# Kernel tuning notes

Measured on AMD Instinct MI355X. Metric: run time of the kernel, lower is better.

Reference implementation:

```python
import jax, jax.numpy as jnp
import numpy as np
from jax import lax

B, H, W, CL, CC, CD, NH, NP = 8, 48, 48, 384, 384, 384, 12, 4
N = H * W
HD = CL // NH
SCALE = HD ** -0.5


def _pool_mat(n, out=7):
    # torch AdaptiveAvgPool2d bin edges: [floor(i*n/out), ceil((i+1)*n/out))
    M = np.zeros((out, n), np.float32)
    for i in range(out):
        s = (i * n) // out
        e = -(-((i + 1) * n) // out)
        M[i, s:e] = 1.0 / (e - s)
    return jnp.asarray(M)


def _resize_mat(out_n, in_n):
    # bilinear, align_corners=False (torch F.interpolate)
    M = np.zeros((out_n, in_n), np.float32)
    scale = in_n / out_n
    for o in range(out_n):
        src = (o + 0.5) * scale - 0.5
        src = min(max(src, 0.0), in_n - 1.0)
        i0 = int(np.floor(src))
        i1 = min(i0 + 1, in_n - 1)
        f = src - i0
        M[o, i0] += 1.0 - f
        M[o, i1] += f
    return jnp.asarray(M)


def _ln_c(x, g, b):
    # LayerNorm over channel dim of NCHW, eps=1e-6
    mu = jnp.mean(x, axis=1, keepdims=True)
    var = jnp.mean((x - mu) ** 2, axis=1, keepdims=True)
    xn = (x - mu) * lax.rsqrt(var + 1e-6)
    return xn * g[None, :, None, None] + b[None, :, None, None]


def _c1(x, w):
    # 1x1 conv, w: (out,in)
    return jnp.einsum('oc,bchw->bohw', w, x)


def _bilerp(feat, grid):
    # feat (G,C,Hs,Ws), grid (G,M,2) xy in [-1,1]; align_corners=False, zero padding
    G, C, Hs, Ws = feat.shape
    x = (grid[..., 0] + 1.0) * 0.5 * Ws - 0.5
    y = (grid[..., 1] + 1.0) * 0.5 * Hs - 0.5
    x0 = jnp.floor(x)
    y0 = jnp.floor(y)
    fx = x - x0
    fy = y - y0
    featf = feat.transpose(0, 2, 3, 1).reshape(G, Hs * Ws, C)
    x0i = x0.astype(jnp.int32)
    y0i = y0.astype(jnp.int32)

    def corner(ix, iy):
        valid = ((ix >= 0) & (ix < Ws) & (iy >= 0) & (iy < Hs)).astype(feat.dtype)
        flat = jnp.clip(iy, 0, Hs - 1) * Ws + jnp.clip(ix, 0, Ws - 1)
        g = jax.vmap(lambda f, i: f[i])(featf, flat)  # (G,M,C)
        return g * valid[..., None]

    v00 = corner(x0i, y0i)
    v01 = corner(x0i + 1, y0i)
    v10 = corner(x0i, y0i + 1)
    v11 = corner(x0i + 1, y0i + 1)
    w00 = ((1 - fx) * (1 - fy))[..., None]
    w01 = (fx * (1 - fy))[..., None]
    w10 = ((1 - fx) * fy)[..., None]
    w11 = (fx * fy)[..., None]
    return v00 * w00 + v01 * w01 + v10 * w10 + v11 * w11  # (G,M,C)


def _forward(local_feat, context_prior, deformable_x, W_q, W_k, W_v, W_pre, ln1_g, ln1_b,
             W_post, dw_w, dw_b, ln2_g, ln2_b, W_lo, b_lo, W_off, b_off,
             attention_biases, W_p, bn_g, bn_b, bn_mean, bn_var):
    q = _c1(local_feat, W_q)  # (B,CL,H,W)

    # context_offset_guide: 1x1 -> GELU -> adaptive pool 7x7 -> LN(C) -> 1x1 to 32 -> resize
    cg = jax.nn.gelu(_c1(context_prior, W_pre), approximate=False)
    Mh, Mw = _pool_mat(H), _pool_mat(W)
    pooled = jnp.einsum('oh,pw,bchw->bcop', Mh, Mw, cg)
    guide = _c1(_ln_c(pooled, ln1_g, ln1_b), W_post)  # (B,32,7,7)
    Uh, Uw = _resize_mat(H, 7), _resize_mat(W, 7)
    guide = jnp.einsum('Oh,Pw,bchw->bcOP', Uh, Uw, guide)  # (B,32,H,W)

    # local_offset_base: dwconv3x3 -> LN(C) -> GELU -> 1x1 to 32
    dw = lax.conv_general_dilated(local_feat, dw_w, (1, 1), [(1, 1), (1, 1)],
                                  dimension_numbers=('NCHW', 'OIHW', 'NCHW'),
                                  feature_group_count=CL) + dw_b[None, :, None, None]
    lo = jax.nn.gelu(_ln_c(dw, ln2_g, ln2_b), approximate=False)
    lo = _c1(lo, W_lo) + b_lo[None, :, None, None]  # (B,32,H,W)

    fused = jnp.concatenate([guide, lo], axis=1)  # (B,64,H,W)
    off = _c1(fused, W_off) + b_off[None, :, None, None]  # (B,NH*NP*2,H,W)
    off = off.transpose(0, 2, 3, 1).reshape(B, H, W, NH, NP, 2)
    offn = off / jnp.asarray([W, H], dtype=off.dtype)

    ry = (jnp.arange(H, dtype=off.dtype) + 0.5) / H
    rx = (jnp.arange(W, dtype=off.dtype) + 0.5) / W
    ref = jnp.stack([jnp.broadcast_to(rx[None, :], (H, W)),
                     jnp.broadcast_to(ry[:, None], (H, W))], axis=-1)  # (H,W,2) xy
    grid = (ref[None, :, :, None, None, :] + offn) * 2.0 - 1.0  # (B,H,W,NH,NP,2)

    gridh = grid.reshape(B, N, NH, NP, 2).transpose(0, 2, 1, 3, 4)  # (B,NH,N,NP,2)
    grid_r = gridh.reshape(B * NH, N * NP, 2)

    k = _c1(context_prior, W_k).reshape(B * NH, HD, H, W)
    v = _c1(deformable_x, W_v).reshape(B * NH, HD, H, W)
    k_s = _bilerp(k, grid_r).reshape(B, NH, N, NP, HD)
    v_s = _bilerp(v, grid_r).reshape(B, NH, N, NP, HD)

    qh = q.reshape(B, NH, HD, N).transpose(0, 1, 3, 2)  # (B,NH,N,HD)
    scores = jnp.einsum('bhnd,bhnpd->bhnp', qh, k_s) * SCALE

    # relative position bias: idx(p1,p2) = |dy|*W + |dx| (first-seen enumeration)
    px = jnp.clip(jnp.round((gridh[..., 0] + 1.0) * 0.5 * W - 0.5), 0, W - 1).astype(jnp.int32)
    py = jnp.clip(jnp.round((gridh[..., 1] + 1.0) * 0.5 * H - 0.5), 0, H - 1).astype(jnp.int32)
    n = jnp.arange(N, dtype=jnp.int32)
    qy = (n // W)[None, None, :, None]
    qx = (n % W)[None, None, :, None]
    bidx = jnp.abs(qy - py) * W + jnp.abs(qx - px)  # (B,NH,N,NP)
    bias = attention_biases[jnp.arange(NH)[None, :, None, None], bidx]

    attn = jax.nn.softmax(scores + bias, axis=-1)
    out = jnp.einsum('bhnp,bhnpd->bhnd', attn, v_s)  # (B,NH,N,HD)
    out = out.transpose(0, 1, 3, 2).reshape(B, CL, H, W)

    y = _c1(out, W_p)
    y = bn_g[None, :, None, None] * (y - bn_mean[None, :, None, None]) * \
        lax.rsqrt(bn_var[None, :, None, None] + 1e-5) + bn_b[None, :, None, None]
    return y


def setup_inputs():
    ks = jax.random.split(jax.random.key(0), 16)
    f32 = jnp.float32
    d = {
        'local_feat': jax.random.normal(ks[0], (B, CL, H, W), f32),
        'context_prior': jax.random.normal(ks[1], (B, CC, H, W), f32),
        'deformable_x': jax.random.normal(ks[2], (B, CD, H, W), f32),
        'W_q': jax.random.normal(ks[3], (CL, CL), f32) * 0.02,
        'W_k': jax.random.normal(ks[4], (CL, CC), f32) * 0.02,
        'W_v': jax.random.normal(ks[5], (CD, CD), f32) * 0.02,
        'W_pre': jax.random.normal(ks[6], (CC, CC), f32) * 0.02,
        'ln1_g': jnp.ones((CC,), f32),
        'ln1_b': jnp.zeros((CC,), f32),
        'W_post': jax.random.normal(ks[7], (32, CC), f32) * 0.02,
        'dw_w': jax.random.normal(ks[8], (CL, 1, 3, 3), f32) * 0.1,
        'dw_b': jnp.zeros((CL,), f32),
        'ln2_g': jnp.ones((CL,), f32),
        'ln2_b': jnp.zeros((CL,), f32),
        'W_lo': jax.random.normal(ks[9], (32, CL), f32) * 0.02,
        'b_lo': jnp.zeros((32,), f32),
        'W_off': jax.random.normal(ks[10], (NH * NP * 2, 64), f32) * 0.01,
        'b_off': jax.random.normal(ks[11], (NH * NP * 2,), f32) * 0.5,
        'attention_biases': jax.random.normal(ks[12], (NH, H * W), f32) * 0.02,
        'W_p': jax.random.normal(ks[13], (CL, CL), f32) * 0.02,
        'bn_g': jnp.ones((CL,), f32),
        'bn_b': jnp.zeros((CL,), f32),
        'bn_mean': jax.random.normal(ks[14], (CL,), f32) * 0.01,
        'bn_var': jax.random.uniform(ks[15], (CL,), f32, 0.5, 1.5),
    }
    return d


def reference(local_feat, context_prior, deformable_x, W_q, W_k, W_v, W_pre, ln1_g, ln1_b,
              W_post, dw_w, dw_b, ln2_g, ln2_b, W_lo, b_lo, W_off, b_off,
              attention_biases, W_p, bn_g, bn_b, bn_mean, bn_var):
    return _forward(local_feat, context_prior, deformable_x, W_q, W_k, W_v, W_pre, ln1_g,
                    ln1_b, W_post, dw_w, dw_b, ln2_g, ln2_b, W_lo, b_lo, W_off, b_off,
                    attention_biases, W_p, bn_g, bn_b, bn_mean, bn_var)
```

## Files before the change

### kernel.cpp

```cpp
#include <hip/hip_runtime.h>
#include <hip/hip_bf16.h>
#include <math.h>

#define B_ 8
#define H_ 48
#define W_ 48
#define N_ 2304
#define C_ 384
#define NH_ 12
#define NP_ 4
#define HD_ 32
#define SCALE_ 0.17677669529663687f

typedef unsigned short ushort;
typedef short bf16x8 __attribute__((ext_vector_type(8)));
typedef float f32x4 __attribute__((ext_vector_type(4)));

__device__ __forceinline__ float b2f(ushort u) {
    union { float f; unsigned i; } x; x.i = ((unsigned)u) << 16; return x.f;
}
__device__ __forceinline__ ushort f2b(float f) {
    __hip_bfloat16 h = __float2bfloat16(f);
    return *(ushort*)&h;
}
__device__ __forceinline__ float ldin(const void* p, size_t i, int isbf) {
    return isbf ? b2f(((const ushort*)p)[i]) : ((const float*)p)[i];
}
__device__ __forceinline__ float geluf(float x) {
    return 0.5f * x * (1.0f + erff(x * 0.70710678118654752440f));
}
__device__ __forceinline__ int iabs(int x) { return x < 0 ? -x : x; }
__device__ __forceinline__ int get_isbf(const void* lnq) {
    return (*(const unsigned*)lnq == 0x3F803F80u) ? 1 : 0;
}

__device__ __forceinline__ void gl_lds16(const ushort* g, ushort* l) {
    __builtin_amdgcn_global_load_lds(
        (const __attribute__((address_space(1))) unsigned int*)g,
        (__attribute__((address_space(3))) unsigned int*)l, 16, 0, 0);
}

#define PREP_MAX 24
struct PrepTab {
    const void* src[PREP_MAX];
    void*       dst[PREP_MAX];
    int         n[PREP_MAX];
    int         tobf[PREP_MAX];
};
struct TPtrs { const void* src[3]; ushort* dst[3]; };
struct SetupRaw {
    const void* WoffRaw;
    const void* WloRaw;
    const void* bloRaw;
    const void* boffRaw;
    const void* dwRaw;
    const void* lnq;
    ushort* Bext;
    float*  biasp;
    float*  dwwT;
};

__global__ __launch_bounds__(256) void setup_kernel(TPtrs tp, PrepTab tab, int ne, SetupRaw rw)
{
    const int isbf = get_isbf(rw.lnq);
    const int tid = threadIdx.x;
    const int bid = blockIdx.x;
    const int DWT0 = ne * 8;
    const int WC0  = DWT0 + 2;
    const int T30  = WC0 + 96;

    if (bid < DWT0) {
        const int e = bid >> 3, sub = bid & 7;
        const int n = tab.n[e];
        const void* src = tab.src[e];
        if (tab.tobf[e]) {
            ushort* dst = (ushort*)tab.dst[e];
            if (isbf) {
                const ushort* s = (const ushort*)src;
                for (int i = sub * 256 + tid; i < n; i += 8 * 256) dst[i] = s[i];
            } else {
                const float* s = (const float*)src;
                for (int i = sub * 256 + tid; i < n; i += 8 * 256) dst[i] = f2b(s[i]);
            }
        } else {
            float* dst = (float*)tab.dst[e];
            if (isbf) {
                const ushort* s = (const ushort*)src;
                for (int i = sub * 256 + tid; i < n; i += 8 * 256) dst[i] = b2f(s[i]);
            } else {
                const float* s = (const float*)src;
                for (int i = sub * 256 + tid; i < n; i += 8 * 256) dst[i] = s[i];
            }
        }
    } else if (bid < WC0) {
        const int c = (bid - DWT0) * 256 + tid;
        if (c < C_) {
#pragma unroll
            for (int u = 0; u < 9; u++)
                rw.dwwT[u * C_ + c] = ldin(rw.dwRaw, (size_t)c * 9 + u, isbf);
        }
    } else if (bid < T30) {
        const int co = bid - WC0;
        for (int c = tid; c < C_; c += 256) {
            float acc = 0.f;
#pragma unroll 8
            for (int j = 0; j < 32; j++)
                acc += ldin(rw.WoffRaw, (size_t)co * 64 + 32 + j, isbf)
                     * ldin(rw.WloRaw, (size_t)j * 384 + c, isbf);
            ushort hi = f2b(acc);
            float r = acc - b2f(hi);
            ushort lo = f2b(r);
            rw.Bext[co * 1152 + c] = hi;
            rw.Bext[co * 1152 + 384 + c] = lo;
            rw.Bext[co * 1152 + 768 + c] = hi;
        }
        if (tid == 0) {
            float bp = ldin(rw.boffRaw, co, isbf);
            for (int j = 0; j < 32; j++)
                bp += ldin(rw.WoffRaw, (size_t)co * 64 + 32 + j, isbf)
                    * ldin(rw.bloRaw, j, isbf);
            rw.biasp[co] = bp;
        }
    } else {
        const int t3 = bid - T30;
        const int x = t3 % 36;
        const int rem = t3 / 36;
        const int y = rem % 12;
        const int z = rem / 12;
        const int which = z >> 3;
        const int b = z & 7;
        const int n0 = x * 64, c0 = y * 32;
        const void* in = tp.src[which];
        ushort* out = tp.dst[which];
        const int t = tid;

        __shared__ unsigned tile[64][33];

        if (isbf) {
            {
                const int c = t >> 3, s = t & 7;
                uint4 v = *(const uint4*)((const ushort*)in + ((size_t)b * C_ + c0 + c) * N_ + n0 + s * 8);
                const int nb = s * 8;
                tile[nb + 0][c] = v.x & 0xffff; tile[nb + 1][c] = v.x >> 16;
                tile[nb + 2][c] = v.y & 0xffff; tile[nb + 3][c] = v.y >> 16;
                tile[nb + 4][c] = v.z & 0xffff; tile[nb + 5][c] = v.z >> 16;
                tile[nb + 6][c] = v.w & 0xffff; tile[nb + 7][c] = v.w >> 16;
            }
            __syncthreads();
            {
                const int n = t >> 2, s = t & 3;
                const int cb = s * 8;
                unsigned p0 = tile[n][cb + 0] | (tile[n][cb + 1] << 16);
                unsigned p1 = tile[n][cb + 2] | (tile[n][cb + 3] << 16);
                unsigned p2 = tile[n][cb + 4] | (tile[n][cb + 5] << 16);
                unsigned p3 = tile[n][cb + 6] | (tile[n][cb + 7] << 16);
                uint4 o; o.x = p0; o.y = p1; o.z = p2; o.w = p3;
                *(uint4*)(out + ((size_t)b * N_ + n0 + n) * C_ + c0 + cb) = o;
            }
        } else {
            float* tf = (float*)&tile[0][0];
            const int tx = t & 31, ty = t >> 5;
            for (int sub = 0; sub < 2; sub++) {
                int ns = n0 + sub * 32;
                __syncthreads();
#pragma unroll
                for (int u = 0; u < 4; u++) {
                    int c = ty + u * 8;
                    tf[c * 33 + tx] = ((const float*)in)[((size_t)b * C_ + c0 + c) * N_ + ns + tx];
                }
                __syncthreads();
#pragma unroll
                for (int u = 0; u < 4; u++) {
                    int n = ty + u * 8;
                    out[((size_t)b * N_ + ns + n) * C_ + c0 + tx] = f2b(tf[tx * 33 + n]);
                }
            }
        }
    }
}

struct QKV4Ptrs { const ushort* A[4]; const ushort* Bw[4]; void* Y[4]; };
__global__ __launch_bounds__(256, 5) void mega_gemm_kernel(
    QKV4Ptrs qp,
    const ushort* __restrict__ AHI, const ushort* __restrict__ ALO,
    const ushort* __restrict__ Bext, float* __restrict__ OFFP)
{
    __shared__ ushort As[2][128 * 32];
    __shared__ ushort Bs[2][128 * 32];
    const int tid = threadIdx.x;
    const int lane = tid & 63, wave = tid >> 6;
    const int wr = wave >> 1, wc = wave & 1;
    const int quad = lane >> 4, l15 = lane & 15;
    const int bid = blockIdx.x;

    if (bid < 144) {
        const int m0 = bid * 128;

        f32x4 acc[4][3];
#pragma unroll
        for (int i = 0; i < 4; i++)
#pragma unroll
            for (int j = 0; j < 3; j++) acc[i][j] = (f32x4){0.f, 0.f, 0.f, 0.f};

        auto stage = [&](int p, int t) {
            const int seg = t / 12;
            const ushort* Ag = (seg < 2) ? AHI : ALO;
            const int acol = t * 32 - seg * 384;
            const int bcol = t * 32;
#pragma unroll
            for (int u = 0; u < 2; u++) {
                int idx = tid + 256 * u;
                int r = idx >> 2, s = idx & 3;
                int rb = r < 96 ? r : 95;
                gl_lds16(Ag + (size_t)(m0 + r) * 384 + acol + 8 * s, &As[p][idx * 8]);
                gl_lds16(Bext + (size_t)rb * 1152 + bcol + 8 * s, &Bs[p][idx * 8]);
            }
        };

        stage(0, 0);
        const int nt = 36;
        for (int t = 0; t < nt; ++t) {
            if (t + 1 < nt) {
                stage((t + 1) & 1, t + 1);
                asm volatile("s_waitcnt vmcnt(4)" ::: "memory");
            } else {
                asm volatile("s_waitcnt vmcnt(0)" ::: "memory");
            }
            __builtin_amdgcn_s_barrier();
            __builtin_amdgcn_sched_barrier(0);
            const int p = t & 1;
            bf16x8 af[4], bfr[3];
#pragma unroll
            for (int i = 0; i < 4; i++)
                af[i]  = *(const bf16x8*)&As[p][(wr * 64 + i * 16 + l15) * 32 + quad * 8];
#pragma unroll
            for (int j = 0; j < 3; j++)
                bfr[j] = *(const bf16x8*)&Bs[p][(wc * 48 + j * 16 + l15) * 32 + quad * 8];
#pragma unroll
            for (int i = 0; i < 4; i++)
#pragma unroll
                for (int j = 0; j < 3; j++)
                    acc[i][j] = __builtin_amdgcn_mfma_f32_16x16x32_bf16(af[i], bfr[j], acc[i][j], 0, 0, 0);
            __builtin_amdgcn_s_barrier();
        }

#pragma unroll
        for (int i = 0; i < 4; i++) {
#pragma unroll
            for (int r = 0; r < 4; r++) {
                int m = m0 + wr * 64 + i * 16 + quad * 4 + r;
#pragma unroll
                for (int j = 0; j < 3; j++) {
                    int co = wc * 48 + j * 16 + l15;
                    OFFP[(size_t)m * 96 + co] = acc[i][j][r];
                }
            }
        }
    } else {
        const int q = bid - 144;
        const int zc = q / 54, r2 = q % 54;
        const int which = zc >> 3, b = zc & 7;
        const int m0 = (r2 / 3) * 128;
        const int n0 = (r2 % 3) * 128;
        const ushort* Ag = qp.A[which];
        const ushort* Bg = qp.Bw[which];

        f32x4 acc[4][4];
#pragma unroll
        for (int i = 0; i < 4; i++)
#pragma unroll
            for (int j = 0; j < 4; j++) acc[i][j] = (f32x4){0.f, 0.f, 0.f, 0.f};

        const size_t abase = (size_t)b * (size_t)N_ * C_;

        auto stage = [&](int p, int kc) {
#pragma unroll
            for (int u = 0; u < 2; u++) {
                int idx = tid + 256 * u;
                int r = idx >> 2, s = idx & 3;
                gl_lds16(Ag + abase + (size_t)(m0 + r) * C_ + kc + 8 * s, &As[p][idx * 8]);
                gl_lds16(Bg + (size_t)(n0 + r) * C_ + kc + 8 * s, &Bs[p][idx * 8]);
            }
        };

        stage(0, 0);
        const int nt = C_ / 32;
        for (int t = 0; t < nt; ++t) {
            if (t + 1 < nt) {
                stage((t + 1) & 1, (t + 1) * 32);
                asm volatile("s_waitcnt vmcnt(4)" ::: "memory");
            } else {
                asm volatile("s_waitcnt vmcnt(0)" ::: "memory");
            }
            __builtin_amdgcn_s_barrier();
            __builtin_amdgcn_sched_barrier(0);
            const int p = t & 1;
            bf16x8 af[4], bfr[4];
#pragma unroll
            for (int i = 0; i < 4; i++)
                af[i]  = *(const bf16x8*)&As[p][(wr * 64 + i * 16 + l15) * 32 + quad * 8];
#pragma unroll
            for (int j = 0; j < 4; j++)
                bfr[j] = *(const bf16x8*)&Bs[p][(wc * 64 + j * 16 + l15) * 32 + quad * 8];
#pragma unroll
            for (int i = 0; i < 4; i++)
#pragma unroll
                for (int j = 0; j < 4; j++)
                    acc[i][j] = __builtin_amdgcn_mfma_f32_16x16x32_bf16(af[i], bfr[j], acc[i][j], 0, 0, 0);
            __builtin_amdgcn_s_barrier();
        }

        ushort* Yg = (ushort*)qp.Y[which];
        if (which < 3) {
#pragma unroll
            for (int i = 0; i < 4; i++) {
#pragma unroll
                for (int r = 0; r < 4; r++) {
                    int m = m0 + wr * 64 + i * 16 + quad * 4 + r;
#pragma unroll
                    for (int j = 0; j < 4; j++) {
                        int nn = n0 + wc * 64 + j * 16 + l15;
                        Yg[abase + (size_t)m * C_ + nn] = f2b(acc[i][j][r]);
                    }
                }
            }
        } else {
#pragma unroll
            for (int i = 0; i < 4; i++) {
#pragma unroll
                for (int r = 0; r < 4; r++) {
                    int m = m0 + wr * 64 + i * 16 + quad * 4 + r;
#pragma unroll
                    for (int j = 0; j < 4; j++) {
                        int nn = n0 + wc * 64 + j * 16 + l15;
                        Yg[abase + (size_t)m * C_ + nn] = f2b(geluf(acc[i][j][r]));
                    }
                }
            }
        }
    }
}

__global__ __launch_bounds__(256) void gemm_final_kernel(
    const ushort* __restrict__ WpB, const ushort* __restrict__ AOut,
    void* __restrict__ Yg,
    const float* __restrict__ bng, const float* __restrict__ bnb,
    const float* __restrict__ bnm, const float* __restrict__ bnv,
    const void* __restrict__ lnq)
{
    const int isbf = get_isbf(lnq);
    const int l = (blockIdx.x & 7) * 108 + (blockIdx.x >> 3);
    const int b = l / 108, r2 = l % 108;
    const int n0 = (r2 / 3) * 64;
    const int m0 = (r2 % 3) * 128;

    __shared__ ushort As[2][128 * 32];
    __shared__ ushort Bs[2][64 * 32];
    const int tid = threadIdx.x;
    const int lane = tid & 63, wave = tid >> 6;
    const int quad = lane >> 4, l15 = lane & 15;
    const int sx = (quad ^ (l15 & 3)) * 8;

    f32x4 acc[2][4];
#pragma unroll
    for (int i = 0; i < 2; i++)
#pragma unroll
        for (int j = 0; j < 4; j++) acc[i][j] = (f32x4){0.f, 0.f, 0.f, 0.f};

    const size_t bbase = (size_t)b * (size_t)N_ * C_;

    auto stage = [&](int p, int kc) {
#pragma unroll
        for (int u = 0; u < 2; u++) {
            int idx = tid + 256 * u;
            int r = idx >> 2, sl = idx & 3;
            int sg = sl ^ (r & 3);
            gl_lds16(WpB + (size_t)(m0 + r) * C_ + kc + 8 * sg, &As[p][idx * 8]);
        }
        {
            int r = tid >> 2, sl = tid & 3;
            int sg = sl ^ (r & 3);
            gl_lds16(AOut + bbase + (size_t)(n0 + r) * C_ + kc + 8 * sg, &Bs[p][tid * 8]);
        }
    };

    stage(0, 0);

    const int nt = C_ / 32;
    for (int t = 0; t < nt; ++t) {
        if (t + 1 < nt) {
            stage((t + 1) & 1, (t + 1) * 32);
            asm volatile("s_waitcnt vmcnt(3)" ::: "memory");
        } else {
            asm volatile("s_waitcnt vmcnt(0)" ::: "memory");
        }
        __builtin_amdgcn_s_barrier();
        __builtin_amdgcn_sched_barrier(0);
        const int p = t & 1;
        bf16x8 af[2], bfr[4];
#pragma unroll
        for (int i = 0; i < 2; i++)
            af[i]  = *(const bf16x8*)&As[p][(wave * 32 + i * 16 + l15) * 32 + sx];
#pragma unroll
        for (int j = 0; j < 4; j++)
            bfr[j] = *(const bf16x8*)&Bs[p][(j * 16 + l15) * 32 + sx];
#pragma unroll
        for (int i = 0; i < 2; i++)
#pragma unroll
            for (int j = 0; j < 4; j++)
                acc[i][j] = __builtin_amdgcn_mfma_f32_16x16x32_bf16(af[i], bfr[j], acc[i][j], 0, 0, 0);
        __builtin_amdgcn_s_barrier();
    }

    const size_t ybase = (size_t)b * (size_t)C_ * N_;
#pragma unroll
    for (int i = 0; i < 2; i++) {
#pragma unroll
        for (int r = 0; r < 4; r++) {
            int m = m0 + wave * 32 + i * 16 + quad * 4 + r;
            float sc = bng[m] * rsqrtf(bnv[m] + 1e-5f);
            float sh = bnb[m] - sc * bnm[m];
#pragma unroll
            for (int j = 0; j < 4; j++) {
                int nn = n0 + j * 16 + l15;
                float v = sc * acc[i][j][r] + sh;
                size_t yi = ybase + (size_t)m * N_ + nn;
                if (isbf) ((ushort*)Yg)[yi] = f2b(v);
                else ((float*)Yg)[yi] = v;
            }
        }
    }
}

__global__ __launch_bounds__(384) void pool_ln_guide_kernel(
    const ushort* __restrict__ CG, const float* __restrict__ g, const float* __restrict__ bt,
    const ushort* __restrict__ WpostB, const ushort* __restrict__ WoffB,
    float* __restrict__ OG7)
{
    const int cell = blockIdx.x % 49, b = blockIdx.x / 49;
    const int i = cell / 7, j = cell % 7, c = threadIdx.x;
    const int sh = (i * H_) / 7, eh = ((i + 1) * H_ + 6) / 7;
    const int sw = (j * W_) / 7, ew = ((j + 1) * W_ + 6) / 7;
    float s = 0.f;
    for (int h = sh; h < eh; h++)
        for (int w = sw; w < ew; w++)
            s += b2f(CG[((size_t)b * N_ + h * W_ + w) * C_ + c]);
    s *= 1.0f / (float)((eh - sh) * (ew - sw));

    float rs = s, rq = s * s;
#pragma unroll
    for (int m = 1; m <= 32; m <<= 1) {
        rs += __shfl_xor(rs, m);
        rq += __shfl_xor(rq, m);
    }
    __shared__ float ss[6], sq[6], buf[C_];
    __shared__ float psum[12][33];
    __shared__ float g7s[32];
    int wid = threadIdx.x >> 6;
    if ((threadIdx.x & 63) == 0) { ss[wid] = rs; sq[wid] = rq; }
    __syncthreads();
    if (threadIdx.x == 0) {
        float ts = 0.f, tq = 0.f;
        for (int k = 0; k < 6; k++) { ts += ss[k]; tq += sq[k]; }
        ss[0] = ts; sq[0] = tq;
    }
    __syncthreads();
    float mu = ss[0] / (float)C_;
    float var = sq[0] / (float)C_ - mu * mu;
    float inv = rsqrtf(var + 1e-6f);
    buf[c] = (s - mu) * inv * g[c] + bt[c];
    __syncthreads();

    const int oc = threadIdx.x & 31, seg = threadIdx.x >> 5;
    const uint4* wp = (const uint4*)(WpostB + oc * C_ + seg * 32);
    float part = 0.f;
#pragma unroll
    for (int u = 0; u < 4; u++) {
        uint4 v = wp[u];
        const float* bb = &buf[seg * 32 + u * 8];
        part += b2f((ushort)(v.x & 0xffff)) * bb[0] + b2f((ushort)(v.x >> 16)) * bb[1];
        part += b2f((ushort)(v.y & 0xffff)) * bb[2] + b2f((ushort)(v.y >> 16)) * bb[3];
        part += b2f((ushort)(v.z & 0xffff)) * bb[4] + b2f((ushort)(v.z >> 16)) * bb[5];
        part += b2f((ushort)(v.w & 0xffff)) * bb[6] + b2f((ushort)(v.w >> 16)) * bb[7];
    }
    psum[seg][oc] = part;
    __syncthreads();
    if (threadIdx.x < 32) {
        float acc = 0.f;
#pragma unroll
        for (int k = 0; k < 12; k++) acc += psum[k][threadIdx.x];
        g7s[threadIdx.x] = acc;
    }
    __syncthreads();
    if (threadIdx.x < 96) {
        const int co = threadIdx.x;
        float acc = 0.f;
#pragma unroll 8
        for (int k = 0; k < 32; k++)
            acc += b2f(WoffB[co * 64 + k]) * g7s[k];
        OG7[(size_t)blockIdx.x * 96 + co] = acc;
    }
}

__global__ __launch_bounds__(512) void dw_ln_gelu_kernel(
    const ushort* __restrict__ LF, const float* __restrict__ WdT, const float* __restrict__ BdF,
    const float* __restrict__ g, const float* __restrict__ bt,
    ushort* __restrict__ AHI, ushort* __restrict__ ALO)
{
    const int wave = threadIdx.x >> 6, lane = threadIdx.x & 63;
    const int m = blockIdx.x * 8 + wave;
    const int b = m / N_, n = m % N_;
    const int h = n / W_, w = n % W_;
    const bool act = lane < 48;
    const int c0 = lane * 8;

    float acc[8];
#pragma unroll
    for (int j = 0; j < 8; j++) acc[j] = 0.f;
    if (act) {
        f32x4 b0 = *(const f32x4*)(BdF + c0);
        f32x4 b1 = *(const f32x4*)(BdF + c0 + 4);
#pragma unroll
        for (int j = 0; j < 4; j++) { acc[j] = b0[j]; acc[4 + j] = b1[j]; }
    }

#pragma unroll
    for (int u = 0; u < 9; u++) {
        const int ky = u / 3, kx = u % 3;
        const int y = h + ky - 1, x = w + kx - 1;
        if (act && y >= 0 && y < H_ && x >= 0 && x < W_) {
            uint4 v = *(const uint4*)(LF + ((size_t)b * N_ + y * W_ + x) * C_ + c0);
            f32x4 wa = *(const f32x4*)(WdT + u * C_ + c0);
            f32x4 wb = *(const f32x4*)(WdT + u * C_ + c0 + 4);
            acc[0] += wa[0] * b2f((ushort)(v.x & 0xffff));
            acc[1] += wa[1] * b2f((ushort)(v.x >> 16));
            acc[2] += wa[2] * b2f((ushort)(v.y & 0xffff));
            acc[3] += wa[3] * b2f((ushort)(v.y >> 16));
            acc[4] += wb[0] * b2f((ushort)(v.z & 0xffff));
            acc[5] += wb[1] * b2f((ushort)(v.z >> 16));
            acc[6] += wb[2] * b2f((ushort)(v.w & 0xffff));
            acc[7] += wb[3] * b2f((ushort)(v.w >> 16));
        }
    }

    float rs = 0.f, rq = 0.f;
#pragma unroll
    for (int j = 0; j < 8; j++) { rs += acc[j]; rq += acc[j] * acc[j]; }
#pragma unroll
    for (int s = 1; s <= 32; s <<= 1) {
        rs += __shfl_xor(rs, s);
        rq += __shfl_xor(rq, s);
    }
    float mu = rs / (float)C_;
    float var = rq / (float)C_ - mu * mu;
    float inv = rsqrtf(var + 1e-6f);

    if (act) {
        f32x4 g0 = *(const f32x4*)(g + c0);
        f32x4 g1 = *(const f32x4*)(g + c0 + 4);
        f32x4 t0 = *(const f32x4*)(bt + c0);
        f32x4 t1 = *(const f32x4*)(bt + c0 + 4);
        float v[8];
#pragma unroll
        for (int j = 0; j < 4; j++) {
            v[j]     = geluf((acc[j]     - mu) * inv * g0[j] + t0[j]);
            v[4 + j] = geluf((acc[4 + j] - mu) * inv * g1[j] + t1[j]);
        }
        uint4 hi, lo;
        ushort hs[8], ls[8];
#pragma unroll
        for (int j = 0; j < 8; j++) {
            hs[j] = f2b(v[j]);
            ls[j] = f2b(v[j] - b2f(hs[j]));
        }
        hi.x = (unsigned)hs[0] | ((unsigned)hs[1] << 16);
        hi.y = (unsigned)hs[2] | ((unsigned)hs[3] << 16);
        hi.z = (unsigned)hs[4] | ((unsigned)hs[5] << 16);
        hi.w = (unsigned)hs[6] | ((unsigned)hs[7] << 16);
        lo.x = (unsigned)ls[0] | ((unsigned)ls[1] << 16);
        lo.y = (unsigned)ls[2] | ((unsigned)ls[3] << 16);
        lo.z = (unsigned)ls[4] | ((unsigned)ls[5] << 16);
        lo.w = (unsigned)ls[6] | ((unsigned)ls[7] << 16);
        size_t idx = (size_t)m * C_ + c0;
        *(uint4*)(AHI + idx) = hi;
        *(uint4*)(ALO + idx) = lo;
    }
}

__global__ __launch_bounds__(384) void attn_kernel(
    const ushort* __restrict__ Q, const ushort* __restrict__ K, const ushort* __restrict__ V,
    const float* __restrict__ OFFP, const float* __restrict__ biasp,
    const float* __restrict__ OG7,
    const float* __restrict__ ABf, ushort* __restrict__ OUT)
{
    const int pairi = blockIdx.x;
    const int b = pairi / (N_ / 2);
    const int n0 = (pairi % (N_ / 2)) * 2;
    const int tid = threadIdx.x;

    __shared__ int   cidxS[96][4];
    __shared__ float cwS[96][4];
    __shared__ float biasS[96];

    if (tid < 96) {
        const int pos = tid / 48, idx = tid % 48;
        const int n = n0 + pos;
        const int h = n / W_, w = n % W_;
        const int nh = idx >> 2, p = idx & 3;
        const int co = nh * 8 + 2 * p;

        const float fs = 7.0f / 48.0f;
        float sy = fminf(fmaxf(((float)h + 0.5f) * fs - 0.5f, 0.f), 6.f);
        float sx = fminf(fmaxf(((float)w + 0.5f) * fs - 0.5f, 0.f), 6.f);
        int gy0 = (int)floorf(sy), gx0 = (int)floorf(sx);
        int gy1 = min(gy0 + 1, 6), gx1 = min(gx0 + 1, 6);
        float gfy = sy - (float)gy0, gfx = sx - (float)gx0;
        float bw00 = (1.f - gfy) * (1.f - gfx), bw01 = (1.f - gfy) * gfx;
        float bw10 = gfy * (1.f - gfx), bw11 = gfy * gfx;
        const float* ogb = OG7 + (size_t)b * 49 * 96;
        int c00 = (gy0 * 7 + gx0) * 96, c01 = (gy0 * 7 + gx1) * 96;
        int c10 = (gy1 * 7 + gx0) * 96, c11 = (gy1 * 7 + gx1) * 96;
        const size_t mrow = ((size_t)b * N_ + n) * 96;

        float ox = OFFP[mrow + co] + biasp[co]
                 + bw00 * ogb[c00 + co] + bw01 * ogb[c01 + co]
                 + bw10 * ogb[c10 + co] + bw11 * ogb[c11 + co];
        float oy = OFFP[mrow + co + 1] + biasp[co + 1]
                 + bw00 * ogb[c00 + co + 1] + bw01 * ogb[c01 + co + 1]
                 + bw10 * ogb[c10 + co + 1] + bw11 * ogb[c11 + co + 1];

        float x = (float)w + ox;
        float y = (float)h + oy;

        int px = (int)fminf(fmaxf(rintf(x), 0.f), (float)(W_ - 1));
        int py = (int)fminf(fmaxf(rintf(y), 0.f), (float)(H_ - 1));
        biasS[tid] = ABf[(size_t)nh * N_ + iabs(h - py) * W_ + iabs(w - px)];

        float x0f = floorf(x), y0f = floorf(y);
        float fx = x - x0f, fy = y - y0f;
        int x0 = (int)x0f, y0 = (int)y0f;
#pragma unroll
        for (int cc = 0; cc < 4; cc++) {
            int dx = cc & 1, dy = cc >> 1;
            int ix = x0 + dx, iy = y0 + dy;
            bool valid = (ix >= 0) && (ix < W_) && (iy >= 0) && (iy < H_);
            int ixc = min(max(ix, 0), W_ - 1), iyc = min(max(iy, 0), H_ - 1);
            cidxS[tid][cc] = iyc * W_ + ixc;
            float wx = dx ? fx : (1.f - fx);
            float wy = dy ? fy : (1.f - fy);
            cwS[tid][cc] = valid ? wx * wy : 0.f;
        }
    }
    __syncthreads();

    const int pos = tid / 192, r = tid % 192;
    const int nh = r >> 4, dd = r & 15;
    const int n = n0 + pos;
    const size_t row = ((size_t)b * N_ + n) * C_ + nh * HD_ + dd * 2;
    unsigned qu = *(const unsigned*)(Q + row);
    const float q0 = b2f((ushort)(qu & 0xffff));
    const float q1 = b2f((ushort)(qu >> 16));
    const size_t kvbase = (size_t)b * N_ * C_ + nh * HD_ + dd * 2;
    const int s0 = pos * 48 + nh * 4;

    int   ci[NP_][4];
    float cw[NP_][4];
#pragma unroll
    for (int p = 0; p < NP_; p++)
#pragma unroll
        for (int cc = 0; cc < 4; cc++) {
            ci[p][cc] = cidxS[s0 + p][cc];
            cw[p][cc] = cwS[s0 + p][cc];
        }

    float sc[NP_];
#pragma unroll
    for (int p = 0; p < NP_; p++) {
        float ks0 = 0.f, ks1 = 0.f;
#pragma unroll
        for (int cc = 0; cc < 4; cc++) {
            unsigned kv = *(const unsigned*)(K + kvbase + (size_t)ci[p][cc] * C_);
            ks0 += cw[p][cc] * b2f((ushort)(kv & 0xffff));
            ks1 += cw[p][cc] * b2f((ushort)(kv >> 16));
        }
        float dot = q0 * ks0 + q1 * ks1;
#pragma unroll
        for (int m = 1; m <= 8; m <<= 1) dot += __shfl_xor(dot, m);
        sc[p] = dot * SCALE_ + biasS[s0 + p];
    }

    float m = fmaxf(fmaxf(sc[0], sc[1]), fmaxf(sc[2], sc[3]));
    float e[NP_], esum = 0.f;
#pragma unroll
    for (int p = 0; p < NP_; p++) { e[p] = __expf(sc[p] - m); esum += e[p]; }
    float inv = 1.0f / esum;

    float o0 = 0.f, o1 = 0.f;
#pragma unroll
    for (int p = 0; p < NP_; p++) {
        float vs0 = 0.f, vs1 = 0.f;
#pragma unroll
        for (int cc = 0; cc < 4; cc++) {
            unsigned vv = *(const unsigned*)(V + kvbase + (size_t)ci[p][cc] * C_);
            vs0 += cw[p][cc] * b2f((ushort)(vv & 0xffff));
            vs1 += cw[p][cc] * b2f((ushort)(vv >> 16));
        }
        float ep = e[p] * inv;
        o0 += ep * vs0;
        o1 += ep * vs1;
    }
    unsigned ou = (unsigned)f2b(o0) | ((unsigned)f2b(o1) << 16);
    *(unsigned*)(OUT + row) = ou;
}

extern "C" void kernel_launch(void* const* d_in, const int* in_sizes, int n_in,
                              void* d_out, int out_size, void* d_ws, size_t ws_size,
                              hipStream_t stream)
{
    const void* local_feat    = d_in[0];
    const void* context_prior = d_in[1];
    const void* deformable_x  = d_in[2];

    const size_t BIGE = (size_t)B_ * N_ * C_;

    char* wsb = (char*)d_ws;
    auto carve = [&](size_t bytes) { char* p = wsb; wsb += (bytes + 255) & ~(size_t)255; return p; };
    int*    flag = (int*)carve(256);
    ushort* T1   = (ushort*)carve(BIGE * 2);
    ushort* T2   = (ushort*)carve(BIGE * 2);
    ushort* T3   = (ushort*)carve(BIGE * 2);
    ushort* Qb   = (ushort*)carve(BIGE * 2);
    ushort* Kb   = (ushort*)carve(BIGE * 2);
    ushort* Vb   = (ushort*)carve(BIGE * 2);
    ushort* AHI  = (ushort*)carve(BIGE * 2);
    ushort* ALO  = (ushort*)carve(BIGE * 2);
    ushort* CGB  = (ushort*)carve(BIGE * 2);
    ushort* AOut = (ushort*)carve(BIGE * 2);
    float*  OFFB = (float*)carve((size_t)B_ * N_ * 96 * 4);
    ushort* WqB   = (ushort*)carve(147456 * 2);
    ushort* WkB   = (ushort*)carve(147456 * 2);
    ushort* WvB   = (ushort*)carve(147456 * 2);
    ushort* WpreB = (ushort*)carve(147456 * 2);
    ushort* WpB   = (ushort*)carve(147456 * 2);
    ushort* WpostB= (ushort*)carve(12288 * 2);
    ushort* WoffB = (ushort*)carve(6144 * 2);
    ushort* Bext  = (ushort*)carve(96 * 1152 * 2);
    float*  biasp = (float*)carve(96 * 4);
    float*  OG7   = (float*)carve((size_t)B_ * 49 * 96 * 4);
    float*  dwwT  = (float*)carve(3456 * 4);
    float*  ABf   = (float*)carve(27648 * 4);
    float*  dwbF  = (float*)carve(384 * 4);
    float*  ln1gF = (float*)carve(384 * 4);
    float*  ln1bF = (float*)carve(384 * 4);
    float*  ln2gF = (float*)carve(384 * 4);
    float*  ln2bF = (float*)carve(384 * 4);
    float*  bngF  = (float*)carve(384 * 4);
    float*  bnbF  = (float*)carve(384 * 4);
    float*  bnmF  = (float*)carve(384 * 4);
    float*  bnvF  = (float*)carve(384 * 4);
    (void)flag;

    PrepTab tab;
    int ne = 0;
    auto add = [&](const void* s, void* d, int n, int tb) {
        tab.src[ne] = s; tab.dst[ne] = d; tab.n[ne] = n; tab.tobf[ne] = tb; ne++;
    };
    add(d_in[3],  WqB,   147456, 1);
    add(d_in[4],  WkB,   147456, 1);
    add(d_in[5],  WvB,   147456, 1);
    add(d_in[6],  WpreB, 147456, 1);
    add(d_in[19], WpB,   147456, 1);
    add(d_in[9],  WpostB, 12288, 1);
    add(d_in[16], WoffB,   6144, 1);
    add(d_in[18], ABf,    27648, 0);
    add(d_in[11], dwbF,     384, 0);
    add(d_in[7],  ln1gF,    384, 0);
    add(d_in[8],  ln1bF,    384, 0);
    add(d_in[12], ln2gF,    384, 0);
    add(d_in[13], ln2bF,    384, 0);
    add(d_in[20], bngF,     384, 0);
    add(d_in[21], bnbF,     384, 0);
    add(d_in[22], bnmF,     384, 0);
    add(d_in[23], bnvF,     384, 0);

    TPtrs tp;
    tp.src[0] = local_feat;    tp.dst[0] = T1;
    tp.src[1] = context_prior; tp.dst[1] = T2;
    tp.src[2] = deformable_x;  tp.dst[2] = T3;

    SetupRaw rw;
    rw.WoffRaw = d_in[16];
    rw.WloRaw  = d_in[14];
    rw.bloRaw  = d_in[15];
    rw.boffRaw = d_in[17];
    rw.dwRaw   = d_in[10];
    rw.lnq     = d_in[7];
    rw.Bext    = Bext;
    rw.biasp   = biasp;
    rw.dwwT    = dwwT;

    const int setup_blocks = ne * 8 + 2 + 96 + 10368;
    setup_kernel<<<setup_blocks, 256, 0, stream>>>(tp, tab, ne, rw);

    dim3 blk256(256);

    dw_ln_gelu_kernel<<<(B_ * N_) / 8, 512, 0, stream>>>(T1, dwwT, dwbF, ln2gF, ln2bF, AHI, ALO);

    QKV4Ptrs qp;
    qp.A[0] = T1; qp.Bw[0] = WqB;   qp.Y[0] = Qb;
    qp.A[1] = T2; qp.Bw[1] = WkB;   qp.Y[1] = Kb;
    qp.A[2] = T3; qp.Bw[2] = WvB;   qp.Y[2] = Vb;
    qp.A[3] = T2; qp.Bw[3] = WpreB; qp.Y[3] = CGB;
    mega_gemm_kernel<<<1872, blk256, 0, stream>>>(qp, AHI, ALO, Bext, OFFB);

    pool_ln_guide_kernel<<<B_ * 49, 384, 0, stream>>>(CGB, ln1gF, ln1bF, WpostB, WoffB, OG7);

    attn_kernel<<<(B_ * N_) / 2, 384, 0, stream>>>(Qb, Kb, Vb, OFFB, biasp, OG7, ABf, AOut);

    gemm_final_kernel<<<864, blk256, 0, stream>>>(
        WpB, AOut, d_out, bngF, bnbF, bnmF, bnvF, d_in[7]);
}
```

Measured before the change: 344.5 us.

## Triple-buffer LDS staging in GEMM kernels and drop trailing barrier

Converts the double-buffered global-to-LDS pipeline in the mega GEMM and final GEMM kernels into a three-stage ring buffer. Two tiles are prefetched ahead, and the next load is issued after the barrier, which lets the second barrier per iteration be removed. The goal is to hide more global load latency and cut synchronization. In exchange, LDS use per block goes up by half and the occupancy hints change (5 to 3 for the mega kernel, 4 added for the final kernel), which may lower the number of resident blocks. A three-deep ring with a single barrier is safe only if no wave is still reading the buffer being overwritten, which holds for distance-2 prefetch.

```diff
diff --git a/kernel.cpp b/kernel.cpp
--- a/kernel.cpp
+++ b/kernel.cpp
@@ -180,13 +180,13 @@
 }
 
 struct QKV4Ptrs { const ushort* A[4]; const ushort* Bw[4]; void* Y[4]; };
-__global__ __launch_bounds__(256, 5) void mega_gemm_kernel(
+__global__ __launch_bounds__(256, 3) void mega_gemm_kernel(
     QKV4Ptrs qp,
     const ushort* __restrict__ AHI, const ushort* __restrict__ ALO,
     const ushort* __restrict__ Bext, float* __restrict__ OFFP)
 {
-    __shared__ ushort As[2][128 * 32];
-    __shared__ ushort Bs[2][128 * 32];
+    __shared__ ushort As[3][128 * 32];
+    __shared__ ushort Bs[3][128 * 32];
     const int tid = threadIdx.x;
     const int lane = tid & 63, wave = tid >> 6;
     const int wr = wave >> 1, wc = wave & 1;
@@ -218,17 +218,15 @@
         };
 
         stage(0, 0);
+        stage(1, 1);
         const int nt = 36;
         for (int t = 0; t < nt; ++t) {
-            if (t + 1 < nt) {
-                stage((t + 1) & 1, t + 1);
-                asm volatile("s_waitcnt vmcnt(4)" ::: "memory");
-            } else {
-                asm volatile("s_waitcnt vmcnt(0)" ::: "memory");
-            }
+            if (t + 1 < nt) asm volatile("s_waitcnt vmcnt(4)" ::: "memory");
+            else            asm volatile("s_waitcnt vmcnt(0)" ::: "memory");
             __builtin_amdgcn_s_barrier();
             __builtin_amdgcn_sched_barrier(0);
-            const int p = t & 1;
+            if (t + 2 < nt) stage((t + 2) % 3, t + 2);
+            const int p = t % 3;
             bf16x8 af[4], bfr[3];
 #pragma unroll
             for (int i = 0; i < 4; i++)
@@ -241,7 +239,6 @@
 #pragma unroll
                 for (int j = 0; j < 3; j++)
                     acc[i][j] = __builtin_amdgcn_mfma_f32_16x16x32_bf16(af[i], bfr[j], acc[i][j], 0, 0, 0);
-            __builtin_amdgcn_s_barrier();
         }
 
 #pragma unroll
@@ -284,17 +281,15 @@
         };
 
         stage(0, 0);
+        stage(1, 32);
         const int nt = C_ / 32;
         for (int t = 0; t < nt; ++t) {
-            if (t + 1 < nt) {
-                stage((t + 1) & 1, (t + 1) * 32);
-                asm volatile("s_waitcnt vmcnt(4)" ::: "memory");
-            } else {
-                asm volatile("s_waitcnt vmcnt(0)" ::: "memory");
-            }
+            if (t + 1 < nt) asm volatile("s_waitcnt vmcnt(4)" ::: "memory");
+            else            asm volatile("s_waitcnt vmcnt(0)" ::: "memory");
             __builtin_amdgcn_s_barrier();
             __builtin_amdgcn_sched_barrier(0);
-            const int p = t & 1;
+            if (t + 2 < nt) stage((t + 2) % 3, (t + 2) * 32);
+            const int p = t % 3;
             bf16x8 af[4], bfr[4];
 #pragma unroll
             for (int i = 0; i < 4; i++)
@@ -307,7 +302,6 @@
 #pragma unroll
                 for (int j = 0; j < 4; j++)
                     acc[i][j] = __builtin_amdgcn_mfma_f32_16x16x32_bf16(af[i], bfr[j], acc[i][j], 0, 0, 0);
-            __builtin_amdgcn_s_barrier();
         }
 
         ushort* Yg = (ushort*)qp.Y[which];
@@ -341,7 +335,7 @@
     }
 }
 
-__global__ __launch_bounds__(256) void gemm_final_kernel(
+__global__ __launch_bounds__(256, 4) void gemm_final_kernel(
     const ushort* __restrict__ WpB, const ushort* __restrict__ AOut,
     void* __restrict__ Yg,
     const float* __restrict__ bng, const float* __restrict__ bnb,
@@ -354,8 +348,8 @@
     const int n0 = (r2 / 3) * 64;
     const int m0 = (r2 % 3) * 128;
 
-    __shared__ ushort As[2][128 * 32];
-    __shared__ ushort Bs[2][64 * 32];
+    __shared__ ushort As[3][128 * 32];
+    __shared__ ushort Bs[3][64 * 32];
     const int tid = threadIdx.x;
     const int lane = tid & 63, wave = tid >> 6;
     const int quad = lane >> 4, l15 = lane & 15;
@@ -385,18 +379,16 @@
     };
 
     stage(0, 0);
+    stage(1, 32);
 
     const int nt = C_ / 32;
     for (int t = 0; t < nt; ++t) {
-        if (t + 1 < nt) {
-            stage((t + 1) & 1, (t + 1) * 32);
-            asm volatile("s_waitcnt vmcnt(3)" ::: "memory");
-        } else {
-            asm volatile("s_waitcnt vmcnt(0)" ::: "memory");
-        }
+        if (t + 1 < nt) asm volatile("s_waitcnt vmcnt(3)" ::: "memory");
+        else            asm volatile("s_waitcnt vmcnt(0)" ::: "memory");
         __builtin_amdgcn_s_barrier();
         __builtin_amdgcn_sched_barrier(0);
-        const int p = t & 1;
+        if (t + 2 < nt) stage((t + 2) % 3, (t + 2) * 32);
+        const int p = t % 3;
         bf16x8 af[2], bfr[4];
 #pragma unroll
         for (int i = 0; i < 2; i++)
@@ -409,7 +401,6 @@
 #pragma unroll
             for (int j = 0; j < 4; j++)
                 acc[i][j] = __builtin_amdgcn_mfma_f32_16x16x32_bf16(af[i], bfr[j], acc[i][j], 0, 0, 0);
-        __builtin_amdgcn_s_barrier();
     }
 
     const size_t ybase = (size_t)b * (size_t)C_ * N_;
```

Result: faster. 331.7 us (-3.7%).
